# Optimization experiments

Hardware: AMD Instinct MI355X
Metric: run time of the kernel (lower is better)

## Reference

```python
import jax, jax.numpy as jnp
import numpy as np

B, T, C, H = 4, 2048, 1024, 16


def setup_inputs() -> dict:
    key = jax.random.key(0)
    k1, k2, k3 = jax.random.split(key, 3)
    x = jax.random.normal(k1, (B, T, C), dtype=jnp.float32)
    Wqkv = jax.random.normal(k2, (C, 3 * C), dtype=jnp.float32) * 0.02
    bqkv = jnp.zeros((3 * C,), dtype=jnp.float32)
    Wproj = jax.random.normal(k3, (C, C), dtype=jnp.float32) * 0.02
    bproj = jnp.zeros((C,), dtype=jnp.float32)
    return {"x": x, "Wqkv": Wqkv, "bqkv": bqkv, "Wproj": Wproj, "bproj": bproj}


def reference(x, Wqkv, bqkv, Wproj, bproj):
    Bx, Tx, Cx = x.shape
    head = Cx // H
    qkv = x @ Wqkv + bqkv                      # [B,T,3C]
    q, k, v = jnp.split(qkv, 3, axis=-1)
    q = q.reshape(Bx, Tx, H, head)
    k = k.reshape(Bx, Tx, H, head)
    v = v.reshape(Bx, Tx, H, head)
    scale = 1.0 / jnp.sqrt(jnp.asarray(head, dtype=x.dtype))
    scores = jnp.einsum('bqhd,bkhd->bhqk', q, k) * scale   # [B,H,T,T]
    causal = jnp.tril(jnp.ones((Tx, Tx), dtype=bool))       # [T,T]
    neg = jnp.finfo(x.dtype).min
    scores = jnp.where(causal[None, None, :, :], scores, neg)
    probs = jax.nn.softmax(scores, axis=-1)
    y = jnp.einsum('bhqk,bkhd->bqhd', probs, v).reshape(Bx, Tx, Cx)
    return y @ Wproj + bproj
```

## Files before the change

### kernel.cpp

```cpp
#include <hip/hip_runtime.h>
#include <stdint.h>

#define BB 4
#define TT 2048
#define CC 1024
#define HH 16

typedef __bf16 bf16x8 __attribute__((ext_vector_type(8)));
typedef float f32x4 __attribute__((ext_vector_type(4)));
typedef float f32x16 __attribute__((ext_vector_type(16)));
typedef unsigned short ushort8 __attribute__((ext_vector_type(8)));
typedef unsigned short ushort4v __attribute__((ext_vector_type(4)));

__device__ __forceinline__ unsigned short f2b(float f) {
    union { float f; unsigned u; } v; v.f = f;
    unsigned r = v.u + 0x7FFFu + ((v.u >> 16) & 1u);
    return (unsigned short)(r >> 16);
}
__device__ __forceinline__ unsigned pack2(float a, float b) {
    union { float f; unsigned u; } ua, ub; ua.f = a; ub.f = b;
    return __builtin_amdgcn_perm(ub.u + 0x8000u, ua.u + 0x8000u, 0x07060302u);
}
__device__ __forceinline__ float fexp2(float x) {
#if __has_builtin(__builtin_amdgcn_exp2f)
    return __builtin_amdgcn_exp2f(x);
#else
    return exp2f(x);
#endif
}
#define LOG2E 1.4426950408889634f

#define ASYNC16(gp, lp) __builtin_amdgcn_global_load_lds( \
    (const __attribute__((address_space(1))) void*)(gp),  \
    (__attribute__((address_space(3))) void*)(lp), 16, 0, 0)

__global__ __launch_bounds__(256) void k_cast(const float* __restrict__ in,
                                              unsigned short* __restrict__ out, int n) {
    int i = (blockIdx.x * 256 + threadIdx.x) * 4;
    if (i >= n) return;
    float4 v = *(const float4*)(in + i);
    ushort4v o;
    o.x = f2b(v.x); o.y = f2b(v.y); o.z = f2b(v.z); o.w = f2b(v.w);
    *(ushort4v*)(out + i) = o;
}

__global__ __launch_bounds__(256) void k_transpose_bf16(const float* __restrict__ in,
                                                        unsigned short* __restrict__ out,
                                                        int R, int Cc) {
    __shared__ float tile[32][33];
    int bx = blockIdx.x * 32, by = blockIdx.y * 32;
    int tx = threadIdx.x, ty = threadIdx.y;
    for (int i = 0; i < 32; i += 8)
        tile[ty + i][tx] = in[(size_t)(by + ty + i) * Cc + bx + tx];
    __syncthreads();
    for (int i = 0; i < 32; i += 8)
        out[(size_t)(bx + ty + i) * R + by + tx] = f2b(tile[tx][ty + i]);
}

#define QSCALE 0.125f

__global__ __launch_bounds__(256, 2) void k_gemmqkv(const unsigned short* __restrict__ A,
                                                    const unsigned short* __restrict__ Bt,
                                                    const float* __restrict__ bias,
                                                    unsigned short* __restrict__ qo,
                                                    unsigned short* __restrict__ ko,
                                                    unsigned short* __restrict__ vo,
                                                    int M, int N, int K) {
    __shared__ unsigned short sm[3 * 12288];
    const int t = threadIdx.x;
    const int lane = t & 63;
    const int c = lane & 15, qd = lane >> 4;
    const int wave = t >> 6;
    const int wr = wave >> 1, wc = wave & 1;
    const int bm = blockIdx.x * 256, bn = blockIdx.y * 128;

    f32x4 acc[8][4] = {};

    const int srow = t >> 2;
    const int sch = (t & 3) ^ ((t >> 3) & 3);
    const unsigned short* Ap = A + (size_t)(bm + srow) * K + sch * 8;
    const unsigned short* Bp = Bt + (size_t)(bn + srow) * K + sch * 8;
    const int fch = qd ^ ((c >> 1) & 3);
    const int NT = K >> 5;

#define STG_P0(buf, tt_) do {                                              \
        const unsigned short* ga_ = Ap + (size_t)(tt_) * 32;               \
        const unsigned short* gb_ = Bp + (size_t)(tt_) * 32;               \
        ASYNC16(ga_,                  &sm[(buf) * 12288 + t * 8]);         \
        ASYNC16(ga_ + (size_t)64 * K, &sm[(buf) * 12288 + 2048 + t * 8]);  \
        ASYNC16(gb_,                  &sm[(buf) * 12288 + 8192 + t * 8]);  \
    } while (0)
#define STG_P1(buf, tt_) do {                                              \
        const unsigned short* ga_ = Ap + (size_t)(tt_) * 32;               \
        const unsigned short* gb_ = Bp + (size_t)(tt_) * 32;               \
        ASYNC16(ga_ + (size_t)128 * K, &sm[(buf) * 12288 + 4096 + t * 8]); \
        ASYNC16(ga_ + (size_t)192 * K, &sm[(buf) * 12288 + 6144 + t * 8]); \
        ASYNC16(gb_ + (size_t)64 * K,  &sm[(buf) * 12288 + 10240 + t * 8]);\
    } while (0)

    STG_P0(0, 0); STG_P1(0, 0);
    STG_P0(1, 1); STG_P1(1, 1);
    asm volatile("s_waitcnt vmcnt(6)" ::: "memory");
    __builtin_amdgcn_s_barrier();

    int bc = 0, b1 = 1, bs = 2;
    for (int tt = 0; tt < NT; ++tt) {
        const unsigned short* Ab = &sm[bc * 12288];
        const unsigned short* Bb = &sm[bc * 12288 + 8192];
        bf16x8 bf_[4], af[4];

        if (tt + 2 < NT) STG_P0(bs, tt + 2);
#pragma unroll
        for (int j = 0; j < 4; j++)
            bf_[j] = *(const bf16x8*)&Bb[(wc * 64 + j * 16 + c) * 32 + fch * 8];
#pragma unroll
        for (int i = 0; i < 4; i++)
            af[i] = *(const bf16x8*)&Ab[(wr * 128 + i * 16 + c) * 32 + fch * 8];
        __builtin_amdgcn_s_barrier();
        asm volatile("s_waitcnt lgkmcnt(0)" ::: "memory");
        __builtin_amdgcn_sched_barrier(0);
        __builtin_amdgcn_s_setprio(1);
#pragma unroll
        for (int i = 0; i < 4; i++)
#pragma unroll
            for (int j = 0; j < 4; j++)
                acc[i][j] = __builtin_amdgcn_mfma_f32_16x16x32_bf16(af[i], bf_[j], acc[i][j], 0, 0, 0);
        __builtin_amdgcn_s_setprio(0);
        __builtin_amdgcn_s_barrier();

        if (tt + 2 < NT) STG_P1(bs, tt + 2);
#pragma unroll
        for (int i = 0; i < 4; i++)
            af[i] = *(const bf16x8*)&Ab[(wr * 128 + 64 + i * 16 + c) * 32 + fch * 8];
        if (tt + 2 < NT) {
            asm volatile("s_waitcnt vmcnt(6)" ::: "memory");
        } else if (tt + 1 < NT) {
            asm volatile("s_waitcnt vmcnt(0)" ::: "memory");
        }
        __builtin_amdgcn_s_barrier();
        asm volatile("s_waitcnt lgkmcnt(0)" ::: "memory");
        __builtin_amdgcn_sched_barrier(0);
        __builtin_amdgcn_s_setprio(1);
#pragma unroll
        for (int i = 0; i < 4; i++)
#pragma unroll
            for (int j = 0; j < 4; j++)
                acc[i + 4][j] = __builtin_amdgcn_mfma_f32_16x16x32_bf16(af[i], bf_[j], acc[i + 4][j], 0, 0, 0);
        __builtin_amdgcn_s_setprio(0);
        __builtin_amdgcn_s_barrier();

        int tmp = bc; bc = b1; b1 = bs; bs = tmp;
    }
#undef STG_P0
#undef STG_P1

#pragma unroll
    for (int j = 0; j < 4; j++) {
        float bv = bias[bn + wc * 64 + j * 16 + c];
#pragma unroll
        for (int i = 0; i < 8; i++)
#pragma unroll
            for (int r = 0; r < 4; r++)
                acc[i][j][r] += bv;
    }

    if (bn < 2048) {
        unsigned short* dst = (bn < 1024) ? qo : ko;
        const int dcol0 = (bn < 1024) ? bn : bn - 1024;
        const float sc = (bn < 1024) ? QSCALE : 1.0f;
        __syncthreads();
#pragma unroll
        for (int i = 0; i < 8; i++) {
            int lr0 = wr * 128 + i * 16 + qd * 4;
#pragma unroll
            for (int j = 0; j < 4; j++) {
                int col = wc * 64 + j * 16 + c;
#pragma unroll
                for (int r = 0; r < 4; r++)
                    sm[(lr0 + r) * 136 + col] = f2b(acc[i][j][r] * sc);
            }
        }
        __syncthreads();
#pragma unroll
        for (int op = 0; op < 16; op++) {
            int cid = op * 256 + t;
            int lr = cid >> 4;
            int ch = (cid & 15) * 8;
            ushort8 v = *(ushort8*)&sm[lr * 136 + ch];
            *(ushort8*)&dst[(size_t)(bm + lr) * 1024 + dcol0 + ch] = v;
        }
    } else {
        const int bseg = bm >> 11;
        const int bmt = bm & 2047;
        __syncthreads();
#pragma unroll
        for (int i = 0; i < 8; i++) {
            int tok = wr * 128 + i * 16 + qd * 4;
#pragma unroll
            for (int j = 0; j < 4; j++) {
                int dl = wc * 64 + j * 16 + c;
                ushort4v pk;
                pk.x = f2b(acc[i][j][0]); pk.y = f2b(acc[i][j][1]);
                pk.z = f2b(acc[i][j][2]); pk.w = f2b(acc[i][j][3]);
                *(ushort4v*)&sm[dl * 264 + tok] = pk;
            }
        }
        __syncthreads();
#pragma unroll
        for (int op = 0; op < 16; op++) {
            int cid = op * 256 + t;
            int dl = cid >> 5;
            int ch = (cid & 31) * 8;
            ushort8 v = *(ushort8*)&sm[dl * 264 + ch];
            int d = (bn - 2048) + dl;
            *(ushort8*)&vo[((size_t)bseg * 1024 + d) * 2048 + bmt + ch] = v;
        }
    }
}

__global__ __launch_bounds__(256, 2) void k_gemmproj(const unsigned short* __restrict__ A,
                                                     const unsigned short* __restrict__ Bt,
                                                     const float* __restrict__ bias,
                                                     float* __restrict__ outf,
                                                     int M, int N, int K) {
    __shared__ unsigned short sm[3 * 8192];
    const int t = threadIdx.x;
    const int lane = t & 63;
    const int c = lane & 15, qd = lane >> 4;
    const int wave = t >> 6;
    const int wr = wave >> 1, wc = wave & 1;
    const int bm = blockIdx.x * 128, bn = blockIdx.y * 128;

    f32x4 acc[4][4] = {};

    const int srow = t >> 2;
    const int sch = (t & 3) ^ ((t >> 3) & 3);
    const unsigned short* Ap = A + (size_t)(bm + srow) * K + sch * 8;
    const unsigned short* Bp = Bt + (size_t)(bn + srow) * K + sch * 8;
    const int fch = qd ^ ((c >> 1) & 3);
    const int NT = K >> 5;

#define PSTG_A(buf, tt_) do {                                              \
        const unsigned short* ga_ = Ap + (size_t)(tt_) * 32;               \
        ASYNC16(ga_,                  &sm[(buf) * 8192 + t * 8]);          \
        ASYNC16(ga_ + (size_t)64 * K, &sm[(buf) * 8192 + 2048 + t * 8]);   \
    } while (0)
#define PSTG_B(buf, tt_) do {                                              \
        const unsigned short* gb_ = Bp + (size_t)(tt_) * 32;               \
        ASYNC16(gb_,                  &sm[(buf) * 8192 + 4096 + t * 8]);   \
        ASYNC16(gb_ + (size_t)64 * K, &sm[(buf) * 8192 + 6144 + t * 8]);   \
    } while (0)

    PSTG_A(0, 0); PSTG_B(0, 0);
    PSTG_A(1, 1); PSTG_B(1, 1);
    asm volatile("s_waitcnt vmcnt(4)" ::: "memory");
    __builtin_amdgcn_s_barrier();

    int bc = 0, b1 = 1, bs = 2;
    for (int tt = 0; tt < NT; ++tt) {
        const unsigned short* Ab = &sm[bc * 8192];
        const unsigned short* Bb = &sm[bc * 8192 + 4096];
        bf16x8 bf_[4], af[2];

        if (tt + 2 < NT) PSTG_A(bs, tt + 2);
#pragma unroll
        for (int j = 0; j < 4; j++)
            bf_[j] = *(const bf16x8*)&Bb[(wc * 64 + j * 16 + c) * 32 + fch * 8];
#pragma unroll
        for (int i = 0; i < 2; i++)
            af[i] = *(const bf16x8*)&Ab[(wr * 64 + i * 16 + c) * 32 + fch * 8];
        __builtin_amdgcn_s_barrier();
        asm volatile("s_waitcnt lgkmcnt(0)" ::: "memory");
        __builtin_amdgcn_sched_barrier(0);
        __builtin_amdgcn_s_setprio(1);
#pragma unroll
        for (int i = 0; i < 2; i++)
#pragma unroll
            for (int j = 0; j < 4; j++)
                acc[i][j] = __builtin_amdgcn_mfma_f32_16x16x32_bf16(af[i], bf_[j], acc[i][j], 0, 0, 0);
        __builtin_amdgcn_s_setprio(0);
        __builtin_amdgcn_s_barrier();

        if (tt + 2 < NT) PSTG_B(bs, tt + 2);
#pragma unroll
        for (int i = 0; i < 2; i++)
            af[i] = *(const bf16x8*)&Ab[(wr * 64 + 32 + i * 16 + c) * 32 + fch * 8];
        if (tt + 2 < NT) {
            asm volatile("s_waitcnt vmcnt(4)" ::: "memory");
        } else if (tt + 1 < NT) {
            asm volatile("s_waitcnt vmcnt(0)" ::: "memory");
        }
        __builtin_amdgcn_s_barrier();
        asm volatile("s_waitcnt lgkmcnt(0)" ::: "memory");
        __builtin_amdgcn_sched_barrier(0);
        __builtin_amdgcn_s_setprio(1);
#pragma unroll
        for (int i = 0; i < 2; i++)
#pragma unroll
            for (int j = 0; j < 4; j++)
                acc[i + 2][j] = __builtin_amdgcn_mfma_f32_16x16x32_bf16(af[i], bf_[j], acc[i + 2][j], 0, 0, 0);
        __builtin_amdgcn_s_setprio(0);
        __builtin_amdgcn_s_barrier();

        int tmp = bc; bc = b1; b1 = bs; bs = tmp;
    }
#undef PSTG_A
#undef PSTG_B

#pragma unroll
    for (int j = 0; j < 4; j++) {
        float bv = bias[bn + wc * 64 + j * 16 + c];
#pragma unroll
        for (int i = 0; i < 4; i++)
#pragma unroll
            for (int r = 0; r < 4; r++)
                acc[i][j][r] += bv;
    }

    float* smf = (float*)sm;
    for (int p = 0; p < 4; p++) {
        __syncthreads();
        int lr0 = wr * 16 + qd * 4;
        for (int j = 0; j < 4; j++) {
            int col = wc * 64 + j * 16 + c;
            for (int r = 0; r < 4; r++)
                smf[(lr0 + r) * 132 + col] = acc[p][j][r];
        }
        __syncthreads();
        for (int op = 0; op < 4; op++) {
            int lr = (t >> 5) + op * 8;
            int ch = (t & 31) * 4;
            float4 v = *(float4*)&smf[lr * 132 + ch];
            int grow = bm + (lr >> 4) * 64 + 16 * p + (lr & 15);
            *(float4*)&outf[(size_t)grow * N + bn + ch] = v;
        }
    }
}

__global__ __launch_bounds__(256, 4) void k_attn(const unsigned short* __restrict__ q16,
                                                 const unsigned short* __restrict__ k16,
                                                 const unsigned short* __restrict__ vT16,
                                                 unsigned short* __restrict__ y16) {
    const int h = blockIdx.y, b = blockIdx.z;
    const int qi = (((int)blockIdx.x + h) & 15) ^ ((b & 1) ? 15 : 0);
    __shared__ unsigned short smem[128 * 72];
    unsigned short* q_s = smem;
    unsigned short* k_s = smem;
    unsigned short* vt_s = smem + 64 * 72;
    const int t = threadIdx.x, lane = t & 63, wave = t >> 6;
    const int l31 = lane & 31, hl = lane >> 5;
    const int wq = wave * 32;

    {
        int row = t >> 1, c32 = (t & 1) * 32;
        const unsigned short* src = q16 + ((size_t)(b * TT + qi * 128 + row)) * CC + h * 64 + c32;
        ushort8 v0 = *(const ushort8*)(src);
        ushort8 v1 = *(const ushort8*)(src + 8);
        ushort8 v2 = *(const ushort8*)(src + 16);
        ushort8 v3 = *(const ushort8*)(src + 24);
        *(ushort8*)&q_s[row * 72 + c32] = v0;
        *(ushort8*)&q_s[row * 72 + c32 + 8] = v1;
        *(ushort8*)&q_s[row * 72 + c32 + 16] = v2;
        *(ushort8*)&q_s[row * 72 + c32 + 24] = v3;
    }
    __syncthreads();
    bf16x8 qf[4];
    for (int s = 0; s < 4; s++)
        qf[s] = *(const bf16x8*)&q_s[(wq + l31) * 72 + s * 16 + hl * 8];

    f32x16 oacc[2] = {};
    float m = -3e38f, l = 0.f;
    const int qmaxw = qi * 128 + wq + 31;
    const int qminw = qi * 128 + wq;
    const int qg = qi * 128 + wq + l31;
    const int jn = 2 * qi + 2;
    const unsigned short* kbase = k16 + (size_t)b * TT * CC + h * 64;
    const unsigned short* vbase = vT16 + (((size_t)b * 16 + h) * 64) * TT;

    const int row = t >> 2, c16 = (t & 3) * 16;
    const unsigned short* ksrc = kbase + (size_t)row * CC + c16;
    const unsigned short* vsrc = vbase + (size_t)row * TT + c16;
    ushort8 ka = *(const ushort8*)ksrc, kb = *(const ushort8*)(ksrc + 8);
    ushort8 va = *(const ushort8*)vsrc, vb = *(const ushort8*)(vsrc + 8);

    for (int j = 0; j < jn; j++) {
        __syncthreads();
        *(ushort8*)&k_s[row * 72 + c16] = ka;
        *(ushort8*)&k_s[row * 72 + c16 + 8] = kb;
        *(ushort8*)&vt_s[row * 72 + c16] = va;
        *(ushort8*)&vt_s[row * 72 + c16 + 8] = vb;
        __syncthreads();
        if (j + 1 < jn) {
            const unsigned short* kn = ksrc + (size_t)(j + 1) * 64 * CC;
            const unsigned short* vn = vsrc + (j + 1) * 64;
            ka = *(const ushort8*)kn; kb = *(const ushort8*)(kn + 8);
            va = *(const ushort8*)vn; vb = *(const ushort8*)(vn + 8);
        }
        if (j * 64 > qmaxw) continue;

        f32x16 sacc[2] = {};
        for (int c2 = 0; c2 < 2; c2++)
            for (int s = 0; s < 4; s++) {
                bf16x8 kf = *(const bf16x8*)&k_s[(c2 * 32 + l31) * 72 + s * 16 + hl * 8];
                sacc[c2] = __builtin_amdgcn_mfma_f32_32x32x16_bf16(kf, qf[s], sacc[c2], 0, 0, 0);
            }

        if (j * 64 + 63 > qminw) {
            for (int c2 = 0; c2 < 2; c2++)
                for (int r = 0; r < 16; r++) {
                    int kvg = j * 64 + c2 * 32 + (r & 3) + 8 * (r >> 2) + 4 * hl;
                    if (kvg > qg) sacc[c2][r] = -1e30f;
                }
        }

        float mx = -1e30f;
        for (int c2 = 0; c2 < 2; c2++)
            for (int r = 0; r < 16; r++) mx = fmaxf(mx, sacc[c2][r]);
        mx = fmaxf(mx, __shfl_xor(mx, 32, 64));
        float mn = fmaxf(m, mx);
        float negmnl = -mn * LOG2E;
        float alpha = fexp2(fmaf(m, LOG2E, negmnl));
        m = mn;
        float sum = 0.f;
        unsigned pg[2][4][2];
        for (int c2 = 0; c2 < 2; c2++)
            for (int g = 0; g < 4; g++) {
                float p0 = fexp2(fmaf(sacc[c2][g * 4 + 0], LOG2E, negmnl));
                float p1 = fexp2(fmaf(sacc[c2][g * 4 + 1], LOG2E, negmnl));
                float p2 = fexp2(fmaf(sacc[c2][g * 4 + 2], LOG2E, negmnl));
                float p3 = fexp2(fmaf(sacc[c2][g * 4 + 3], LOG2E, negmnl));
                sum += (p0 + p1) + (p2 + p3);
                pg[c2][g][0] = pack2(p0, p1);
                pg[c2][g][1] = pack2(p2, p3);
            }
        sum += __shfl_xor(sum, 32, 64);
        l = l * alpha + sum;
        if (__ballot(alpha != 1.0f)) {
            for (int c2 = 0; c2 < 2; c2++)
                for (int r = 0; r < 16; r++) oacc[c2][r] *= alpha;
        }

        bf16x8 pf[4];
        for (int c2 = 0; c2 < 2; c2++)
            for (int pr = 0; pr < 2; pr++) {
                unsigned se0 = hl ? pg[c2][2 * pr][0] : pg[c2][2 * pr + 1][0];
                unsigned se1 = hl ? pg[c2][2 * pr][1] : pg[c2][2 * pr + 1][1];
                unsigned r0 = (unsigned)__shfl_xor((int)se0, 32, 64);
                unsigned r1 = (unsigned)__shfl_xor((int)se1, 32, 64);
                union { unsigned u[4]; bf16x8 v; } fr;
                fr.u[0] = hl ? r0 : pg[c2][2 * pr][0];
                fr.u[1] = hl ? r1 : pg[c2][2 * pr][1];
                fr.u[2] = hl ? pg[c2][2 * pr + 1][0] : r0;
                fr.u[3] = hl ? pg[c2][2 * pr + 1][1] : r1;
                pf[c2 * 2 + pr] = fr.v;
            }

        for (int s = 0; s < 4; s++)
            for (int c2o = 0; c2o < 2; c2o++) {
                bf16x8 vf = *(const bf16x8*)&vt_s[(c2o * 32 + l31) * 72 + s * 16 + hl * 8];
                oacc[c2o] = __builtin_amdgcn_mfma_f32_32x32x16_bf16(vf, pf[s], oacc[c2o], 0, 0, 0);
            }
    }

    float rl = 1.0f / l;
    size_t rowb = ((size_t)b * TT + qg) * CC + h * 64;
    for (int c2 = 0; c2 < 2; c2++)
        for (int g = 0; g < 4; g++) {
            ushort4v pk;
            pk.x = f2b(oacc[c2][g * 4 + 0] * rl);
            pk.y = f2b(oacc[c2][g * 4 + 1] * rl);
            pk.z = f2b(oacc[c2][g * 4 + 2] * rl);
            pk.w = f2b(oacc[c2][g * 4 + 3] * rl);
            *(ushort4v*)&y16[rowb + c2 * 32 + g * 8 + hl * 4] = pk;
        }
}

extern "C" void kernel_launch(void* const* d_in, const int* in_sizes, int n_in,
                              void* d_out, int out_size, void* d_ws, size_t ws_size,
                              hipStream_t stream) {
    const float* x     = (const float*)d_in[0];
    const float* Wqkv  = (const float*)d_in[1];
    const float* bqkv  = (const float*)d_in[2];
    const float* Wproj = (const float*)d_in[3];
    const float* bproj = (const float*)d_in[4];
    float* out = (float*)d_out;

    const int M = BB * TT;
    unsigned short* x16    = (unsigned short*)d_ws;
    unsigned short* y16    = x16;
    unsigned short* wqkvT  = x16 + (size_t)M * CC;
    unsigned short* wprojT = wqkvT + (size_t)3 * CC * CC;
    unsigned short* q16    = wprojT + (size_t)CC * CC;
    unsigned short* k16    = q16 + (size_t)M * CC;
    unsigned short* vT16   = k16 + (size_t)M * CC;

    k_cast<<<(M * CC) / 1024, 256, 0, stream>>>(x, x16, M * CC);
    k_transpose_bf16<<<dim3(3 * CC / 32, CC / 32), dim3(32, 8), 0, stream>>>(Wqkv, wqkvT, CC, 3 * CC);
    k_transpose_bf16<<<dim3(CC / 32, CC / 32), dim3(32, 8), 0, stream>>>(Wproj, wprojT, CC, CC);
    k_gemmqkv<<<dim3(M / 256, 3 * CC / 128), 256, 0, stream>>>(x16, wqkvT, bqkv,
                                                               q16, k16, vT16, M, 3 * CC, CC);
    k_attn<<<dim3(TT / 128, HH, BB), 256, 0, stream>>>(q16, k16, vT16, y16);
    k_gemmproj<<<dim3(M / 128, CC / 128), 256, 0, stream>>>(y16, wprojT, bproj, out, M, CC, CC);
}
```

Before: 247.9 us.

## Pair complementary causal query tiles per attention block to share K/V loads

Each attention block now runs 512 threads covering two query tiles, qi and 15-qi, so every block does the same amount of causal work and the K/V tiles staged in shared memory serve both tiles. K and V loading is split across the two thread halves, and the grid shrinks to half as many blocks. This targets causal load imbalance and redundant K/V global reads. The cost is larger blocks, a larger shared buffer and a loop length set by the longer tile, so waves on the shorter tile sit idle at barriers for the later iterations.

```diff
diff --git a/kernel.cpp b/kernel.cpp
--- a/kernel.cpp
+++ b/kernel.cpp
@@ -337,23 +337,29 @@
     }
 }
 
-__global__ __launch_bounds__(256, 4) void k_attn(const unsigned short* __restrict__ q16,
+__global__ __launch_bounds__(512, 4) void k_attn(const unsigned short* __restrict__ q16,
                                                  const unsigned short* __restrict__ k16,
                                                  const unsigned short* __restrict__ vT16,
                                                  unsigned short* __restrict__ y16) {
     const int h = blockIdx.y, b = blockIdx.z;
-    const int qi = (((int)blockIdx.x + h) & 15) ^ ((b & 1) ? 15 : 0);
-    __shared__ unsigned short smem[128 * 72];
+    const int u = ((int)blockIdx.x + h) & 7;
+    const int base = ((b >> 1) & 1) ? 7 - u : u;
+    const int qiA = base, qiB = 15 - base;
+    __shared__ unsigned short smem[256 * 72];
     unsigned short* q_s = smem;
     unsigned short* k_s = smem;
     unsigned short* vt_s = smem + 64 * 72;
     const int t = threadIdx.x, lane = t & 63, wave = t >> 6;
     const int l31 = lane & 31, hl = lane >> 5;
-    const int wq = wave * 32;
+    const int tile = wave >> 2;
+    const int qw = (wave & 3) * 32;
+    const int qi = tile ? qiB : qiA;
 
     {
         int row = t >> 1, c32 = (t & 1) * 32;
-        const unsigned short* src = q16 + ((size_t)(b * TT + qi * 128 + row)) * CC + h * 64 + c32;
+        int qtile = row >> 7, rr = row & 127;
+        int qsrc_i = qtile ? qiB : qiA;
+        const unsigned short* src = q16 + ((size_t)(b * TT + qsrc_i * 128 + rr)) * CC + h * 64 + c32;
         ushort8 v0 = *(const ushort8*)(src);
         ushort8 v1 = *(const ushort8*)(src + 8);
         ushort8 v2 = *(const ushort8*)(src + 16);
@@ -366,35 +372,34 @@
     __syncthreads();
     bf16x8 qf[4];
     for (int s = 0; s < 4; s++)
-        qf[s] = *(const bf16x8*)&q_s[(wq + l31) * 72 + s * 16 + hl * 8];
+        qf[s] = *(const bf16x8*)&q_s[(tile * 128 + qw + l31) * 72 + s * 16 + hl * 8];
 
     f32x16 oacc[2] = {};
     float m = -3e38f, l = 0.f;
-    const int qmaxw = qi * 128 + wq + 31;
-    const int qminw = qi * 128 + wq;
-    const int qg = qi * 128 + wq + l31;
-    const int jn = 2 * qi + 2;
+    const int qmaxw = qi * 128 + qw + 31;
+    const int qminw = qi * 128 + qw;
+    const int qg = qi * 128 + qw + l31;
+    const int jn = 2 * qiB + 2;
     const unsigned short* kbase = k16 + (size_t)b * TT * CC + h * 64;
     const unsigned short* vbase = vT16 + (((size_t)b * 16 + h) * 64) * TT;
 
-    const int row = t >> 2, c16 = (t & 3) * 16;
-    const unsigned short* ksrc = kbase + (size_t)row * CC + c16;
-    const unsigned short* vsrc = vbase + (size_t)row * TT + c16;
-    ushort8 ka = *(const ushort8*)ksrc, kb = *(const ushort8*)(ksrc + 8);
-    ushort8 va = *(const ushort8*)vsrc, vb = *(const ushort8*)(vsrc + 8);
+    const int t2 = t & 255;
+    const int row = t2 >> 2, c16 = (t2 & 3) * 16;
+    const bool doK = (t < 256);
+    const unsigned short* ssrc = (doK ? (kbase + (size_t)row * CC)
+                                      : (vbase + (size_t)row * TT)) + c16;
+    unsigned short* sdst = (doK ? k_s : vt_s) + row * 72 + c16;
+    const size_t sstep = doK ? (size_t)64 * CC : (size_t)64;
+    ushort8 sa = *(const ushort8*)ssrc, sb = *(const ushort8*)(ssrc + 8);
 
     for (int j = 0; j < jn; j++) {
         __syncthreads();
-        *(ushort8*)&k_s[row * 72 + c16] = ka;
-        *(ushort8*)&k_s[row * 72 + c16 + 8] = kb;
-        *(ushort8*)&vt_s[row * 72 + c16] = va;
-        *(ushort8*)&vt_s[row * 72 + c16 + 8] = vb;
+        *(ushort8*)sdst = sa;
+        *(ushort8*)(sdst + 8) = sb;
         __syncthreads();
         if (j + 1 < jn) {
-            const unsigned short* kn = ksrc + (size_t)(j + 1) * 64 * CC;
-            const unsigned short* vn = vsrc + (j + 1) * 64;
-            ka = *(const ushort8*)kn; kb = *(const ushort8*)(kn + 8);
-            va = *(const ushort8*)vn; vb = *(const ushort8*)(vn + 8);
+            const unsigned short* nx = ssrc + (size_t)(j + 1) * sstep;
+            sa = *(const ushort8*)nx; sb = *(const ushort8*)(nx + 8);
         }
         if (j * 64 > qmaxw) continue;
 
@@ -499,6 +504,6 @@
     k_transpose_bf16<<<dim3(CC / 32, CC / 32), dim3(32, 8), 0, stream>>>(Wproj, wprojT, CC, CC);
     k_gemmqkv<<<dim3(M / 256, 3 * CC / 128), 256, 0, stream>>>(x16, wqkvT, bqkv,
                                                                q16, k16, vT16, M, 3 * CC, CC);
-    k_attn<<<dim3(TT / 128, HH, BB), 256, 0, stream>>>(q16, k16, vT16, y16);
+    k_attn<<<dim3(8, HH, BB), 512, 0, stream>>>(q16, k16, vT16, y16);
     k_gemmproj<<<dim3(M / 128, CC / 128), 256, 0, stream>>>(y16, wprojT, bproj, out, M, CC, CC);
 }
```

After: 245.5 us. Within noise of the previous version (-1.0%).
